# Performance work log

Hardware: AMD Instinct MI355X
Metric: run time of the kernel (lower is better)

## Reference

```python
import jax, jax.numpy as jnp
import numpy as np

B, NCH, T = 16, 64, 15000
WS, ST = 500, 250
SR = 250.0
EPS = 1e-06
DM = 512
LN_EPS = 1e-05


def _spectral_constants():
    freqs = np.fft.rfftfreq(WS, d=1.0 / SR).astype(np.float32)  # [F]
    bands = [(1.0, 4.0), (4.0, 8.0), (8.0, 13.0), (13.0, 30.0)]
    bm = np.stack([(freqs >= lo) & (freqs < hi) for lo, hi in bands]).astype(np.float32)  # [4, F]
    bm_norm = bm / bm.sum(axis=1, keepdims=True)  # mean over band bins == matmul with normalized mask
    alpha = ((freqs >= 7.0) & (freqs <= 13.5)).astype(np.float32)  # [F]
    return jnp.asarray(freqs), jnp.asarray(bm_norm), jnp.asarray(alpha)

FREQS, BAND_MASK_NORM, ALPHA_MASK = _spectral_constants()
NUM_FRAMES = (T - WS) // ST + 1
FRAME_IDX = np.arange(NUM_FRAMES)[:, None] * ST + np.arange(WS)[None, :]  # [W, WS]


def _linear_params(k, fin, fout):
    kw, kb = jax.random.split(k)
    W = jax.random.normal(kw, (fin, fout), jnp.float32) * 0.02
    b = jax.random.normal(kb, (fout,), jnp.float32) * 0.01
    return W, b


def setup_inputs() -> dict:
    key = jax.random.key(0)
    ks = jax.random.split(key, 8)
    x = jax.random.normal(ks[0], (B, NCH, T), jnp.float32)
    sensor_pos = jax.random.normal(ks[1], (B, NCH, 2), jnp.float32) * 0.1
    sensor_mask = jax.random.bernoulli(ks[2], 0.9, (B, NCH))
    IN_F = 4 * 3 + 3   # 15
    IN_D = 4 * 2 + 3   # 11
    Wf1, bf1 = _linear_params(ks[3], IN_F, DM)
    Wf2, bf2 = _linear_params(ks[4], DM, DM)
    Wd1, bd1 = _linear_params(ks[5], IN_D, DM)
    Wd2, bd2 = _linear_params(ks[6], DM, DM)
    ln_g = jnp.ones((DM,), jnp.float32)
    ln_b = jnp.zeros((DM,), jnp.float32)
    return {"x": x, "sensor_pos": sensor_pos, "sensor_mask": sensor_mask,
            "Wf1": Wf1, "bf1": bf1, "Wf2": Wf2, "bf2": bf2,
            "ln_g": ln_g, "ln_b": ln_b,
            "Wd1": Wd1, "bd1": bd1, "Wd2": Wd2, "bd2": bd2}


def _mlp(z, W1, b1, W2, b2):
    h = jax.nn.gelu(z @ W1 + b1, approximate=False)
    return h @ W2 + b2


def _layernorm(z, g, b):
    mu = z.mean(-1, keepdims=True)
    var = jnp.var(z, axis=-1, keepdims=True)
    return (z - mu) * jax.lax.rsqrt(var + LN_EPS) * g + b


def _safe_mask(v, fallback):
    return jnp.where(v.any(), v, jnp.full_like(v, fallback))


def _forward(x, sensor_pos, sensor_mask, Wf1, bf1, Wf2, bf2, ln_g, ln_b, Wd1, bd1, Wd2, bd2):
    # frames: [B, W, C, WS]
    frames = x[:, :, FRAME_IDX].transpose(0, 2, 1, 3)
    frames = frames - frames.mean(-1, keepdims=True)
    valid = sensor_mask.astype(frames.dtype)[:, None, :, None]  # [B,1,C,1]
    frames = frames * valid
    spec = jnp.fft.rfft(frames.astype(jnp.float32), axis=-1)
    power = jnp.abs(spec) ** 2 + EPS  # [B,W,C,F]

    # masked band-power means via normalized mask matmul -> [B,W,C,4]
    band_power_t = jnp.einsum('bwcf,kf->bwck', power, BAND_MASK_NORM)
    total_power = jnp.maximum(band_power_t.sum(-1, keepdims=True), EPS)
    rel_power = band_power_t / total_power

    valid_ch = valid  # [B,1,C,1]
    ch_cnt = jnp.maximum(valid_ch.sum(2, keepdims=True), 1.0)
    chan_mean = (band_power_t * valid_ch).sum(2, keepdims=True) / ch_cnt
    topo_dev = jnp.log(jnp.maximum(band_power_t, EPS)) - jnp.log(jnp.maximum(chan_mean, EPS))

    pos_x = sensor_pos[..., 0]
    pos_y = sensor_pos[..., 1]
    left = _safe_mask((pos_x < -0.02) & sensor_mask, False)
    right = _safe_mask((pos_x > 0.02) & sensor_mask, False)
    posterior = _safe_mask((pos_y < -0.02) & sensor_mask, True)
    anterior = _safe_mask((pos_y > 0.02) & sensor_mask, False)

    alpha_power = band_power_t[..., 2]  # [B,W,C]

    def region_mean(m):  # m: [B,C] bool -> [B,W]
        cnt = jnp.maximum(m.sum(-1).astype(alpha_power.dtype), 1.0)[:, None]
        return (alpha_power * m.astype(alpha_power.dtype)[:, None, :]).sum(-1) / cnt

    left_a, right_a = region_mean(left), region_mean(right)
    post_a, ant_a = region_mean(posterior), region_mean(anterior)
    alpha_asym = (left_a - right_a) / jnp.maximum(left_a + right_a + EPS, EPS)
    alpha_ap = (post_a - ant_a) / jnp.maximum(post_a + ant_a + EPS, EPS)
    support = (anterior.sum(-1) > 0) & (posterior.sum(-1) > 0)  # [B]
    alpha_ap = jnp.where(support[:, None], alpha_ap, jnp.zeros_like(alpha_ap))

    alpha_spec = power * ALPHA_MASK  # [B,W,C,F]
    alpha_sum = jnp.maximum(alpha_spec.sum(-1), EPS)
    alpha_peak_freq = (alpha_spec * FREQS).sum(-1) / alpha_sum  # [B,W,C]
    alpha_peak_score = alpha_spec.max(-1) / jnp.maximum(power.mean(-1), EPS)

    log_power = jnp.log(jnp.maximum(band_power_t, EPS))
    channel_ap = jnp.broadcast_to(sensor_pos[:, None, :, 1], alpha_peak_freq.shape)

    features = jnp.concatenate([
        log_power, rel_power, topo_dev,
        alpha_peak_freq[..., None], alpha_peak_score[..., None], channel_ap[..., None],
    ], axis=-1)  # [B,W,C,15]

    ch_cnt2 = jnp.maximum(valid_ch.sum(2), 1.0)  # [B,1,1]
    band_mean = (band_power_t * valid_ch).sum(2) / ch_cnt2       # [B,W,4]
    band_rel_mean = (rel_power * valid_ch).sum(2) / ch_cnt2      # [B,W,4]
    band_log_mean = jnp.log(jnp.maximum(band_mean, EPS))
    delta_theta = band_rel_mean[..., 0] + band_rel_mean[..., 1]
    desc = jnp.concatenate([
        band_log_mean, band_rel_mean,
        jnp.stack([alpha_asym, alpha_ap, delta_theta], axis=-1),
    ], axis=-1)  # [B,W,11]

    tokens = _layernorm(_mlp(features.astype(x.dtype), Wf1, bf1, Wf2, bf2), ln_g, ln_b)
    desc_out = _mlp(desc.astype(x.dtype), Wd1, bd1, Wd2, bd2)
    return tokens, desc_out


def reference(x, sensor_pos, sensor_mask, Wf1, bf1, Wf2, bf2, ln_g, ln_b, Wd1, bd1, Wd2, bd2):
    return _forward(x, sensor_pos, sensor_mask, Wf1, bf1, Wf2, bf2, ln_g, ln_b, Wd1, bd1, Wd2, bd2)
```

## Files before the change

### kernel.cpp

```cpp
#include <hip/hip_runtime.h>
#include <math.h>

#define EPS 1e-6f
#define LN_EPS 1e-5f

typedef __attribute__((ext_vector_type(8))) short bf16x8;
typedef __attribute__((ext_vector_type(4))) float f32x4;

#define SD_OFF    0ULL
#define SD_SZ     (1024ULL*60*128*4)
#define BP_OFF    SD_OFF
#define BTH_OFF   (SD_OFF + 4ULL*1024*1024)
#define BTL_OFF   (BTH_OFF + 65536ULL)
#define FEAT_OFF  (SD_OFF + SD_SZ)
#define FEAT_SZ   (60416ULL*16*4)
#define W1H_OFF   (FEAT_OFF + FEAT_SZ)
#define W1L_OFF   (W1H_OFF + 32768ULL)
#define WT_OFF    (W1L_OFF + 32768ULL)
#define WT_SZ     (512ULL*512*2)
#define DSC_OFF   (WT_OFF + WT_SZ)
#define DSC_SZ    (944ULL*16*4)
#define MSK_OFF   (DSC_OFF + DSC_SZ)
#define MSK_SZ    (1024ULL*4)
#define REG_OFF   (MSK_OFF + MSK_SZ)
#define REG_SZ    (4096ULL*4)
#define CNT_OFF   (REG_OFF + REG_SZ)
#define CNT_SZ    (64ULL*4)
#define SUP_OFF   (CNT_OFF + CNT_SZ)

#define TOKENS_N  30932992ULL

__device__ inline unsigned short f2bf(float f) {
  union { float f; unsigned u; } v; v.f = f;
  unsigned u = v.u;
  return (unsigned short)((u + 0x7fffu + ((u >> 16) & 1u)) >> 16);
}

__device__ inline void gload16(const void* g, void* l) {
  __builtin_amdgcn_global_load_lds((const __attribute__((address_space(1))) unsigned int*)g,
                                   (__attribute__((address_space(3))) unsigned int*)l, 16, 0, 0);
}

__global__ __launch_bounds__(1024) void k_setup(const void* mraw, const float* spos,
    float* maskf, float* regm, float* cnts, float* sup) {
  __shared__ int okint, okflt;
  __shared__ int anyr[4];
  __shared__ float cbuf[4][16];
  int t = threadIdx.x;
  if (t == 0) { okint = 1; okflt = 1; }
  if (t < 4) anyr[t] = 0;
  if (t < 64) cbuf[t>>4][t&15] = 0.f;
  __syncthreads();
  if (t < 256) {
    unsigned v = ((const unsigned*)mraw)[t];
    if (v > 1u) okint = 0;
    if (v != 0u && v != 0x3f800000u) okflt = 0;
  }
  __syncthreads();
  float mv;
  if (okint)      mv = (float)((const int*)mraw)[t];
  else if (okflt) mv = ((const float*)mraw)[t];
  else            mv = (float)((const unsigned char*)mraw)[t];
  maskf[t] = mv;
  bool mk = mv > 0.5f;
  float px = spos[2*t], py = spos[2*t+1];
  int lm = ((px < -0.02f) && mk) ? 1 : 0;
  int rm = ((px >  0.02f) && mk) ? 1 : 0;
  int pm = ((py < -0.02f) && mk) ? 1 : 0;
  int am = ((py >  0.02f) && mk) ? 1 : 0;
  if (lm) anyr[0] = 1;
  if (rm) anyr[1] = 1;
  if (pm) anyr[2] = 1;
  if (am) anyr[3] = 1;
  __syncthreads();
  float lv = anyr[0] ? (float)lm : 0.f;
  float rv = anyr[1] ? (float)rm : 0.f;
  float pv = anyr[2] ? (float)pm : 1.f;
  float av = anyr[3] ? (float)am : 0.f;
  regm[t] = lv; regm[1024+t] = rv; regm[2048+t] = pv; regm[3072+t] = av;
  int b = t >> 6;
  atomicAdd(&cbuf[0][b], lv);
  atomicAdd(&cbuf[1][b], rv);
  atomicAdd(&cbuf[2][b], pv);
  atomicAdd(&cbuf[3][b], av);
  __syncthreads();
  if (t < 64) cnts[t] = cbuf[t>>4][t&15];
  if (t < 16) sup[t] = (cbuf[3][t] > 0.f && cbuf[2][t] > 0.f) ? 1.f : 0.f;
}

__global__ __launch_bounds__(256) void k_wt(const float* Wf2, unsigned short* Wt) {
  __shared__ float tile[64][65];
  int tx = threadIdx.x & 63, ty = threadIdx.x >> 6;
  int k0 = blockIdx.x * 64, n0 = blockIdx.y * 64;
  for (int r = ty; r < 64; r += 4)
    tile[r][tx] = Wf2[(size_t)(k0 + r)*512 + n0 + tx];
  __syncthreads();
  for (int r = ty; r < 64; r += 4)
    Wt[(size_t)(n0 + r)*512 + k0 + tx] = f2bf(tile[tx][r]);
}

__global__ __launch_bounds__(256) void k_w1(const float* Wf1, unsigned short* W1h, unsigned short* W1l) {
  int id = blockIdx.x*256 + threadIdx.x;
  int col = id & 511, k = id >> 9;
  float w = (k < 15) ? Wf1[k*512 + col] : 0.f;
  unsigned u = __float_as_uint(w);
  float hf = __uint_as_float(u & 0xffff0000u);
  float r = w - hf;
  int idx = (((col >> 4)*4 + (k >> 3))*16 + (col & 15))*8 + (k & 7);
  W1h[idx] = (unsigned short)(u >> 16);
  W1l[idx] = (unsigned short)(__float_as_uint(r) >> 16);
}

__global__ __launch_bounds__(256) void k_twid(unsigned short* FBh, unsigned short* FBl) {
  int col = blockIdx.x, k = threadIdx.x;
  float w = 0.f;
  if (k < 250) {
    if (col < 116) {
      int kk = (col >> 1) + 2;
      int km = (kk * k) % 500;
      float ang = (float)km * 0.012566370614359172f;
      w = (col & 1) ? sinf(ang) : cosf(ang);
    } else if (col == 116) w = (k & 1) ? -1.f : 1.f;
    else if (col == 117) w = 1.f;
  }
  unsigned u = __float_as_uint(w);
  float hf = __uint_as_float(u & 0xffff0000u);
  float r = w - hf;
  int ni2 = col >> 6, nf = (col >> 4) & 3, r15 = col & 15;
  int kt = k >> 5, lg4 = (k >> 3) & 3, e = k & 7;
  int idx = ((((kt*2 + ni2)*4 + nf)*64) + (lg4*16 + r15))*8 + e;
  FBh[idx] = (unsigned short)(u >> 16);
  FBl[idx] = (unsigned short)(__float_as_uint(r) >> 16);
}

__global__ __launch_bounds__(256) void k_dft(const float* __restrict__ x, const float* maskf,
    const unsigned short* __restrict__ FBh, const unsigned short* __restrict__ FBl,
    float* __restrict__ bpg) {
  int c = blockIdx.x, b = blockIdx.y;
  int bc = b*64 + c;
  __shared__ __align__(16) float xs[15360];
  __shared__ float Ep[64][4];
  int t = threadIdx.x;
  float mvv = maskf[bc];
  const float4* xp4 = (const float4*)(x + (size_t)bc*15000);
  float4* xs4 = (float4*)xs;
  for (int i = t; i < 3750; i += 256) {
    float4 v = xp4[i];
    v.x *= mvv; v.y *= mvv; v.z *= mvv; v.w *= mvv;
    xs4[i] = v;
  }
  if (t < 90) xs4[3750 + t] = make_float4(0.f, 0.f, 0.f, 0.f);
  __syncthreads();
  if (t < 240) {
    int j = t >> 2, q = t & 3;
    int len = (q < 3) ? 31 : 32;
    const float2* p = (const float2*)(xs + j*250 + q*62);
    float e = 0.f;
    for (int i = 0; i < len; ++i) { float2 v = p[i]; e = fmaf(v.x, v.x, fmaf(v.y, v.y, e)); }
    Ep[j][q] = e;
  }
  int L = t & 63, wv = t >> 6;
  int mi2 = wv >> 1, ni2 = wv & 1;
  int r15 = L & 15, lg4 = L >> 4;
  f32x4 acc[2][4];
#pragma unroll
  for (int mf = 0; mf < 2; ++mf)
#pragma unroll
    for (int nf = 0; nf < 4; ++nf) acc[mf][nf] = (f32x4){0.f,0.f,0.f,0.f};
  int rowA = mi2*32 + r15;
  const unsigned short* fbh0 = FBh + (size_t)(ni2*4*64 + L)*8;
  const unsigned short* fbl0 = FBl + (size_t)(ni2*4*64 + L)*8;
  for (int kt = 0; kt < 8; ++kt) {
    int k0 = kt*32 + lg4*8;
    bf16x8 bh[4], bl[4];
#pragma unroll
    for (int nf = 0; nf < 4; ++nf) {
      bh[nf] = *(const bf16x8*)(fbh0 + (size_t)(kt*8 + nf)*512);
      bl[nf] = *(const bf16x8*)(fbl0 + (size_t)(kt*8 + nf)*512);
    }
    bf16x8 ah[2], al[2];
#pragma unroll
    for (int mf = 0; mf < 2; ++mf) {
      int row = rowA + mf*16;
      if (row > 60) row = 60;
      int base = row*250 + k0;
      float v[8];
#pragma unroll
      for (int p = 0; p < 4; ++p) {
        float2 vv = *(const float2*)(xs + base + 2*p);
        v[2*p] = vv.x; v[2*p+1] = vv.y;
      }
#pragma unroll
      for (int e = 0; e < 8; ++e) {
        unsigned u = __float_as_uint(v[e]);
        float hf = __uint_as_float(u & 0xffff0000u);
        ah[mf][e] = (short)(u >> 16);
        al[mf][e] = (short)(__float_as_uint(v[e] - hf) >> 16);
      }
    }
#pragma unroll
    for (int mf = 0; mf < 2; ++mf)
#pragma unroll
      for (int nf = 0; nf < 4; ++nf) {
        acc[mf][nf] = __builtin_amdgcn_mfma_f32_16x16x32_bf16(ah[mf], bh[nf], acc[mf][nf], 0, 0, 0);
        acc[mf][nf] = __builtin_amdgcn_mfma_f32_16x16x32_bf16(al[mf], bh[nf], acc[mf][nf], 0, 0, 0);
        acc[mf][nf] = __builtin_amdgcn_mfma_f32_16x16x32_bf16(ah[mf], bl[nf], acc[mf][nf], 0, 0, 0);
      }
  }
  __syncthreads();
  float* Ts = xs;
#pragma unroll
  for (int mf = 0; mf < 2; ++mf)
#pragma unroll
    for (int nf = 0; nf < 4; ++nf) {
      int col = ni2*64 + nf*16 + r15;
      int rw = mi2*32 + mf*16 + lg4*4;
#pragma unroll
      for (int q = 0; q < 4; ++q) Ts[(rw + q)*129 + col] = acc[mf][nf][q];
    }
  __syncthreads();
  if (t < 59) {
    int w = t;
    const float* r0 = Ts + w*129;
    const float* r1 = Ts + (w+1)*129;
    float bs0=0,bs1=0,bs2=0,bs3=0, asum=0, afsum=0, amax=0;
#pragma unroll
    for (int i = 0; i < 58; ++i) {
      float sg = (i & 1) ? -1.f : 1.f;
      float tc = fmaf(sg, r1[2*i],   r0[2*i]);
      float ts = fmaf(sg, r1[2*i+1], r0[2*i+1]);
      float P = fmaf(tc, tc, fmaf(ts, ts, EPS));
      if (i < 6) bs0 += P; else if (i < 14) bs1 += P; else if (i < 24) bs2 += P; else bs3 += P;
      if (i >= 12 && i <= 25) { asum += P; afsum = fmaf(P, 0.5f*(float)(i+2), afsum); amax = fmaxf(amax, P); }
    }
    float nyq  = r0[116] + r1[116];
    float ssum = r0[117] + r1[117];
    float en = Ep[w][0]+Ep[w][1]+Ep[w][2]+Ep[w][3] + Ep[w+1][0]+Ep[w+1][1]+Ep[w+1][2]+Ep[w+1][3];
    float E = fmaf(-ssum * (1.f/500.f), ssum, en);
    float pmean = fmaxf(fmaf(500.f, E, nyq*nyq) * (1.f/502.f) + EPS, EPS);
    float bp0 = bs0*(1.f/6.f), bp1 = bs1*(1.f/8.f), bp2 = bs2*(1.f/10.f), bp3 = bs3*(1.f/34.f);
    float afreq  = afsum / fmaxf(asum, EPS);
    float ascore = amax / pmean;
    float4* o = (float4*)(bpg + (((size_t)(b*59 + w))*64 + c)*8);
    o[0] = make_float4(bp0, bp1, bp2, bp3);
    o[1] = make_float4(afreq, ascore, 0.f, 0.f);
  }
}

__global__ __launch_bounds__(64) void k_feat2(const float* __restrict__ bpg, const float* spos,
    const float* maskf, const float* regm, const float* cnts, const float* sup,
    float* feat, float* descb) {
  int w = blockIdx.x, b = blockIdx.y;
  int c = threadIdx.x, bc = b*64 + c;
  size_t bw = (size_t)(b*59 + w);
  const float4* ip = (const float4*)(bpg + (bw*64 + c)*8);
  float4 f0 = ip[0], f1 = ip[1];
  float bp0 = f0.x, bp1 = f0.y, bp2 = f0.z, bp3 = f0.w;
  float tot = fmaxf(bp0+bp1+bp2+bp3, EPS);
  float rl0 = bp0/tot, rl1 = bp1/tot, rl2 = bp2/tot, rl3 = bp3/tot;
  float valid = maskf[bc];
  float vcnt = valid;
  float ch0 = bp0*valid, ch1 = bp1*valid, ch2 = bp2*valid, ch3 = bp3*valid;
  float br0 = rl0*valid, br1 = rl1*valid, br2 = rl2*valid, br3 = rl3*valid;
  float rg0 = bp2*regm[bc], rg1 = bp2*regm[1024+bc], rg2 = bp2*regm[2048+bc], rg3 = bp2*regm[3072+bc];
#pragma unroll
  for (int off = 1; off < 64; off <<= 1) {
    vcnt += __shfl_xor(vcnt, off, 64);
    ch0 += __shfl_xor(ch0, off, 64); ch1 += __shfl_xor(ch1, off, 64);
    ch2 += __shfl_xor(ch2, off, 64); ch3 += __shfl_xor(ch3, off, 64);
    br0 += __shfl_xor(br0, off, 64); br1 += __shfl_xor(br1, off, 64);
    br2 += __shfl_xor(br2, off, 64); br3 += __shfl_xor(br3, off, 64);
    rg0 += __shfl_xor(rg0, off, 64); rg1 += __shfl_xor(rg1, off, 64);
    rg2 += __shfl_xor(rg2, off, 64); rg3 += __shfl_xor(rg3, off, 64);
  }
  float ccnt = fmaxf(vcnt, 1.f);
  float cm0 = ch0/ccnt, cm1 = ch1/ccnt, cm2 = ch2/ccnt, cm3 = ch3/ccnt;
  float lcm0 = logf(fmaxf(cm0,EPS)), lcm1 = logf(fmaxf(cm1,EPS));
  float lcm2 = logf(fmaxf(cm2,EPS)), lcm3 = logf(fmaxf(cm3,EPS));
  float lg0 = logf(fmaxf(bp0,EPS)), lg1 = logf(fmaxf(bp1,EPS));
  float lg2 = logf(fmaxf(bp2,EPS)), lg3 = logf(fmaxf(bp3,EPS));
  float* fr = feat + (bw*64 + c)*16;
  fr[0]=lg0; fr[1]=lg1; fr[2]=lg2; fr[3]=lg3;
  fr[4]=rl0; fr[5]=rl1; fr[6]=rl2; fr[7]=rl3;
  fr[8]=lg0-lcm0; fr[9]=lg1-lcm1; fr[10]=lg2-lcm2; fr[11]=lg3-lcm3;
  fr[12]=f1.x;
  fr[13]=f1.y;
  fr[14]=spos[bc*2 + 1];
  fr[15]=0.f;
  if (c == 0) {
    float bR0 = br0/ccnt, bR1 = br1/ccnt, bR2 = br2/ccnt, bR3 = br3/ccnt;
    float Lm = rg0 / fmaxf(cnts[b],      1.f);
    float Rm = rg1 / fmaxf(cnts[16+b],   1.f);
    float Pm = rg2 / fmaxf(cnts[32+b],   1.f);
    float Am = rg3 / fmaxf(cnts[48+b],   1.f);
    float* dr = descb + bw*16;
    dr[0]=lcm0; dr[1]=lcm1; dr[2]=lcm2; dr[3]=lcm3;
    dr[4]=bR0; dr[5]=bR1; dr[6]=bR2; dr[7]=bR3;
    dr[8]=(Lm - Rm) / fmaxf(Lm + Rm + EPS, EPS);
    dr[9]=(sup[b] > 0.5f) ? (Pm - Am) / fmaxf(Pm + Am + EPS, EPS) : 0.f;
    dr[10]=bR0 + bR1;
  }
}

__global__ __launch_bounds__(256, 2) void k_tok(const float* __restrict__ feat,
    const unsigned short* __restrict__ W1h, const unsigned short* __restrict__ W1l,
    const float* __restrict__ bf1, const unsigned short* __restrict__ Wt,
    const float* bf2, const float* lng, const float* lnb, float* out) {
  __shared__ __align__(16) unsigned short As[64*32];
  __shared__ __align__(16) unsigned short Bs[512*32];
  __shared__ float b1s[512];
  __shared__ float red[64][4][2];
  __shared__ float lnp[64][2];
  int t = threadIdx.x;
  int L = t & 63, wvid = t >> 6;
  int row0 = blockIdx.x * 64;
  int r15 = L & 15, lg4 = L >> 4;
  if (t < 256) { b1s[t] = bf1[t]; b1s[256+t] = bf1[256+t]; }
  bf16x8 a1h = (bf16x8){0,0,0,0,0,0,0,0}, a1l = (bf16x8){0,0,0,0,0,0,0,0};
  {
    int row = row0 + wvid*16 + r15;
    if (lg4 < 2) {
      const float4* fp = (const float4*)(feat + (size_t)row*16 + lg4*8);
      float4 v0 = fp[0], v1 = fp[1];
      float v[8] = {v0.x, v0.y, v0.z, v0.w, v1.x, v1.y, v1.z, v1.w};
#pragma unroll
      for (int e = 0; e < 8; ++e) {
        unsigned u = __float_as_uint(v[e]);
        float hf = __uint_as_float(u & 0xffff0000u);
        a1h[e] = (short)(u >> 16);
        a1l[e] = (short)(__float_as_uint(v[e] - hf) >> 16);
      }
    }
  }
  f32x4 acc[4][8];
#pragma unroll
  for (int m = 0; m < 4; ++m)
#pragma unroll
    for (int n = 0; n < 8; ++n) acc[m][n] = (f32x4){0.f,0.f,0.f,0.f};
  int swz = (r15 >> 1) & 3;
  int kca = lg4 ^ swz;
  int aoff = r15*32 + kca*8;
  int boff = (wvid*128 + r15)*32 + kca*8;
  __syncthreads();
  for (int kt = 0; kt < 16; ++kt) {
#pragma unroll
    for (int r = 0; r < 8; ++r) {
      int n = r*256 + t;
      int col = n >> 2;
      int kc = (n & 3) ^ ((n >> 3) & 3);
      gload16(Wt + (size_t)col*512 + kt*32 + kc*8, (char*)Bs + n*16);
    }
    f32x4 acc1[2];
    acc1[0] = (f32x4){0.f,0.f,0.f,0.f};
    acc1[1] = (f32x4){0.f,0.f,0.f,0.f};
#pragma unroll
    for (int n2 = 0; n2 < 2; ++n2) {
      const unsigned short* wb = W1h + (size_t)(kt*2 + n2)*512 + L*8;
      const unsigned short* wl = W1l + (size_t)(kt*2 + n2)*512 + L*8;
      bf16x8 b1h = *(const bf16x8*)wb;
      bf16x8 b1l = *(const bf16x8*)wl;
      acc1[n2] = __builtin_amdgcn_mfma_f32_16x16x32_bf16(a1h, b1h, acc1[n2], 0, 0, 0);
      acc1[n2] = __builtin_amdgcn_mfma_f32_16x16x32_bf16(a1l, b1h, acc1[n2], 0, 0, 0);
      acc1[n2] = __builtin_amdgcn_mfma_f32_16x16x32_bf16(a1h, b1l, acc1[n2], 0, 0, 0);
    }
    unsigned short hv[8];
#pragma unroll
    for (int n2 = 0; n2 < 2; ++n2) {
      float bb = b1s[kt*32 + n2*16 + r15];
#pragma unroll
      for (int q = 0; q < 4; ++q) {
        float z = acc1[n2][q] + bb;
        float g = 0.5f * z * (1.f + erff(z * 0.70710678118654752f));
        hv[n2*4 + q] = f2bf(g);
      }
    }
#pragma unroll
    for (int n2 = 0; n2 < 2; ++n2) {
      int col5 = n2*16 + r15;
      int cb = col5 >> 3;
#pragma unroll
      for (int q = 0; q < 4; ++q) {
        int rw = wvid*16 + lg4*4 + q;
        int kcs = cb ^ ((rw >> 1) & 3);
        As[rw*32 + kcs*8 + (col5 & 7)] = hv[n2*4 + q];
      }
    }
    __syncthreads();
    bf16x8 av[4], bv[8];
#pragma unroll
    for (int m = 0; m < 4; ++m) av[m] = *(const bf16x8*)&As[aoff + m*512];
#pragma unroll
    for (int n = 0; n < 8; ++n) bv[n] = *(const bf16x8*)&Bs[boff + n*512];
#pragma unroll
    for (int m = 0; m < 4; ++m)
#pragma unroll
      for (int n = 0; n < 8; ++n)
        acc[m][n] = __builtin_amdgcn_mfma_f32_16x16x32_bf16(av[m], bv[n], acc[m][n], 0, 0, 0);
    __syncthreads();
  }
  float b2v[8], gv[8], btv[8];
#pragma unroll
  for (int n = 0; n < 8; ++n) {
    int col = wvid*128 + n*16 + r15;
    b2v[n] = bf2[col]; gv[n] = lng[col]; btv[n] = lnb[col];
  }
  float s1[4][4], s2[4][4];
#pragma unroll
  for (int m = 0; m < 4; ++m)
#pragma unroll
    for (int r = 0; r < 4; ++r) { s1[m][r] = 0.f; s2[m][r] = 0.f; }
#pragma unroll
  for (int m = 0; m < 4; ++m)
#pragma unroll
    for (int n = 0; n < 8; ++n)
#pragma unroll
      for (int r = 0; r < 4; ++r) {
        float z = acc[m][n][r] + b2v[n];
        acc[m][n][r] = z;
        s1[m][r] += z;
        s2[m][r] = fmaf(z, z, s2[m][r]);
      }
#pragma unroll
  for (int off = 1; off < 16; off <<= 1)
#pragma unroll
    for (int m = 0; m < 4; ++m)
#pragma unroll
      for (int r = 0; r < 4; ++r) {
        s1[m][r] += __shfl_xor(s1[m][r], off, 64);
        s2[m][r] += __shfl_xor(s2[m][r], off, 64);
      }
  if (r15 == 0) {
#pragma unroll
    for (int m = 0; m < 4; ++m)
#pragma unroll
      for (int r = 0; r < 4; ++r) {
        int rw = m*16 + lg4*4 + r;
        red[rw][wvid][0] = s1[m][r];
        red[rw][wvid][1] = s2[m][r];
      }
  }
  __syncthreads();
  if (t < 64) {
    float a = red[t][0][0] + red[t][1][0] + red[t][2][0] + red[t][3][0];
    float q = red[t][0][1] + red[t][1][1] + red[t][2][1] + red[t][3][1];
    float mu = a * (1.f/512.f);
    float var = q * (1.f/512.f) - mu*mu;
    lnp[t][0] = mu;
    lnp[t][1] = rsqrtf(var + LN_EPS);
  }
  __syncthreads();
  float* ob = out + (size_t)row0*512;
#pragma unroll
  for (int m = 0; m < 4; ++m)
#pragma unroll
    for (int r = 0; r < 4; ++r) {
      int rw = m*16 + lg4*4 + r;
      float mu = lnp[rw][0], rs = lnp[rw][1];
#pragma unroll
      for (int n = 0; n < 8; ++n) {
        int col = wvid*128 + n*16 + r15;
        ob[(size_t)rw*512 + col] = fmaf((acc[m][n][r] - mu)*rs, gv[n], btv[n]);
      }
    }
}

__global__ __launch_bounds__(256) void k_desc(const float* descb, const float* Wd1, const float* bd1,
    const float* Wd2, const float* bd2, float* out) {
  int blk = blockIdx.x;
  int cq = blockIdx.y;
  __shared__ float ds[16][12];
  __shared__ float hd[16*512];
  int t = threadIdx.x;
  { int r = t >> 4, cc = t & 15;
    if (cc < 11) ds[r][cc] = descb[(size_t)(blk*16 + r)*16 + cc]; }
  __syncthreads();
  {
    int c0 = t, c1 = t + 256;
    float wa[11], wb[11];
#pragma unroll
    for (int k = 0; k < 11; ++k) { wa[k] = Wd1[k*512+c0]; wb[k] = Wd1[k*512+c1]; }
    float ba = bd1[c0], bb = bd1[c1];
    for (int r = 0; r < 16; ++r) {
      float a0 = ba, a1 = bb;
#pragma unroll
      for (int k = 0; k < 11; ++k) { float f = ds[r][k]; a0 = fmaf(f, wa[k], a0); a1 = fmaf(f, wb[k], a1); }
      hd[r*512+c0] = 0.5f * a0 * (1.f + erff(a0 * 0.70710678118654752f));
      hd[r*512+c1] = 0.5f * a1 * (1.f + erff(a1 * 0.70710678118654752f));
    }
  }
  __syncthreads();
  int col = cq*128 + (t & 127);
  int half = t >> 7;
  float accv[8];
  float bz = bd2[col];
#pragma unroll
  for (int r = 0; r < 8; ++r) accv[r] = bz;
  for (int k4 = 0; k4 < 128; ++k4) {
    float w0 = Wd2[(size_t)(k4*4+0)*512 + col];
    float w1 = Wd2[(size_t)(k4*4+1)*512 + col];
    float w2 = Wd2[(size_t)(k4*4+2)*512 + col];
    float w3 = Wd2[(size_t)(k4*4+3)*512 + col];
#pragma unroll
    for (int r = 0; r < 8; ++r) {
      float4 hv = *(const float4*)&hd[(half*8+r)*512 + k4*4];
      accv[r] = fmaf(hv.x, w0, fmaf(hv.y, w1, fmaf(hv.z, w2, fmaf(hv.w, w3, accv[r]))));
    }
  }
  float* ob = out + TOKENS_N;
#pragma unroll
  for (int r = 0; r < 8; ++r) {
    int grow = blk*16 + half*8 + r;
    ob[(size_t)grow*512 + col] = accv[r];
  }
}

extern "C" void kernel_launch(void* const* d_in, const int* in_sizes, int n_in,
                              void* d_out, int out_size, void* d_ws, size_t ws_size,
                              hipStream_t stream) {
  (void)in_sizes; (void)n_in; (void)out_size; (void)ws_size;
  const float* x    = (const float*)d_in[0];
  const float* spos = (const float*)d_in[1];
  const void*  mask = d_in[2];
  const float* Wf1  = (const float*)d_in[3];
  const float* bf1  = (const float*)d_in[4];
  const float* Wf2  = (const float*)d_in[5];
  const float* bf2  = (const float*)d_in[6];
  const float* lng  = (const float*)d_in[7];
  const float* lnb  = (const float*)d_in[8];
  const float* Wd1  = (const float*)d_in[9];
  const float* bd1  = (const float*)d_in[10];
  const float* Wd2  = (const float*)d_in[11];
  const float* bd2  = (const float*)d_in[12];
  char* ws = (char*)d_ws;
  float*          bpg   = (float*)(ws + BP_OFF);
  unsigned short* FBh   = (unsigned short*)(ws + BTH_OFF);
  unsigned short* FBl   = (unsigned short*)(ws + BTL_OFF);
  float*          feat  = (float*)(ws + FEAT_OFF);
  unsigned short* W1h   = (unsigned short*)(ws + W1H_OFF);
  unsigned short* W1l   = (unsigned short*)(ws + W1L_OFF);
  unsigned short* Wt    = (unsigned short*)(ws + WT_OFF);
  float*          descb = (float*)(ws + DSC_OFF);
  float*          maskf = (float*)(ws + MSK_OFF);
  float*          regm  = (float*)(ws + REG_OFF);
  float*          cnts  = (float*)(ws + CNT_OFF);
  float*          sup   = (float*)(ws + SUP_OFF);
  float*          out   = (float*)d_out;

  hipLaunchKernelGGL(k_setup,  dim3(1),      dim3(1024), 0, stream, mask, spos, maskf, regm, cnts, sup);
  hipLaunchKernelGGL(k_wt,     dim3(8,8),    dim3(256),  0, stream, Wf2, Wt);
  hipLaunchKernelGGL(k_w1,     dim3(64),     dim3(256),  0, stream, Wf1, W1h, W1l);
  hipLaunchKernelGGL(k_twid,   dim3(128),    dim3(256),  0, stream, FBh, FBl);
  hipLaunchKernelGGL(k_dft,    dim3(64,16),  dim3(256),  0, stream, x, maskf, FBh, FBl, bpg);
  hipLaunchKernelGGL(k_feat2,  dim3(59,16),  dim3(64),   0, stream, bpg, spos, maskf, regm, cnts, sup, feat, descb);
  hipLaunchKernelGGL(k_tok,    dim3(944),    dim3(256),  0, stream, feat, W1h, W1l, bf1, Wt, bf2, lng, lnb, out);
  hipLaunchKernelGGL(k_desc,   dim3(59,4),   dim3(256),  0, stream, descb, Wd1, bd1, Wd2, bd2, out);
}
```

Baseline: 345.3 us.

## Split k_tok into producer/consumer waves and use fast erf approximation for GELU

k_tok now runs 512 threads per block: four waves compute the first-layer MLP and GELU into LDS, while the other four issue the Wt global-to-LDS loads. Then all eight waves share the second GEMM as a 2x4 wave grid, so each wave holds half as many accumulators. GELU's erff is replaced by an Abramowitz-Stegun polynomial with a hardware reciprocal and exp, in both k_tok and k_desc. This aims to cut register pressure, raise occupancy and overlap loads with compute, at the cost of a small accuracy loss in GELU.

```diff
diff --git a/kernel.cpp b/kernel.cpp
--- a/kernel.cpp
+++ b/kernel.cpp
@@ -39,6 +39,16 @@
 __device__ inline void gload16(const void* g, void* l) {
   __builtin_amdgcn_global_load_lds((const __attribute__((address_space(1))) unsigned int*)g,
                                    (__attribute__((address_space(3))) unsigned int*)l, 16, 0, 0);
+}
+
+__device__ inline float gelu_f(float z) {
+  float s = z * 0.70710678118654752f;
+  float a = fabsf(s);
+  float t = __builtin_amdgcn_rcpf(fmaf(0.3275911f, a, 1.f));
+  float p = t*(0.254829592f + t*(-0.284496736f + t*(1.421413741f + t*(-1.453152027f + t*1.061405429f))));
+  float e = __expf(-a*a);
+  float er = copysignf(fmaf(-p, e, 1.f), s);
+  return 0.5f * z * (1.f + er);
 }
 
 __global__ __launch_bounds__(1024) void k_setup(const void* mraw, const float* spos,
@@ -302,7 +312,7 @@
   }
 }
 
-__global__ __launch_bounds__(256, 2) void k_tok(const float* __restrict__ feat,
+__global__ __launch_bounds__(512, 4) void k_tok(const float* __restrict__ feat,
     const unsigned short* __restrict__ W1h, const unsigned short* __restrict__ W1l,
     const float* __restrict__ bf1, const unsigned short* __restrict__ Wt,
     const float* bf2, const float* lng, const float* lnb, float* out) {
@@ -312,87 +322,85 @@
   __shared__ float red[64][4][2];
   __shared__ float lnp[64][2];
   int t = threadIdx.x;
-  int L = t & 63, wvid = t >> 6;
+  int L = t & 63, wv = t >> 6;
+  int wm = wv >> 2, wn = wv & 3;
   int row0 = blockIdx.x * 64;
   int r15 = L & 15, lg4 = L >> 4;
-  if (t < 256) { b1s[t] = bf1[t]; b1s[256+t] = bf1[256+t]; }
+  if (t < 512) b1s[t] = bf1[t];
   bf16x8 a1h = (bf16x8){0,0,0,0,0,0,0,0}, a1l = (bf16x8){0,0,0,0,0,0,0,0};
-  {
-    int row = row0 + wvid*16 + r15;
-    if (lg4 < 2) {
-      const float4* fp = (const float4*)(feat + (size_t)row*16 + lg4*8);
-      float4 v0 = fp[0], v1 = fp[1];
-      float v[8] = {v0.x, v0.y, v0.z, v0.w, v1.x, v1.y, v1.z, v1.w};
-#pragma unroll
-      for (int e = 0; e < 8; ++e) {
-        unsigned u = __float_as_uint(v[e]);
-        float hf = __uint_as_float(u & 0xffff0000u);
-        a1h[e] = (short)(u >> 16);
-        a1l[e] = (short)(__float_as_uint(v[e] - hf) >> 16);
-      }
-    }
-  }
-  f32x4 acc[4][8];
-#pragma unroll
-  for (int m = 0; m < 4; ++m)
+  if (wv < 4 && lg4 < 2) {
+    int row = row0 + wv*16 + r15;
+    const float4* fp = (const float4*)(feat + (size_t)row*16 + lg4*8);
+    float4 v0 = fp[0], v1 = fp[1];
+    float v[8] = {v0.x, v0.y, v0.z, v0.w, v1.x, v1.y, v1.z, v1.w};
+#pragma unroll
+    for (int e = 0; e < 8; ++e) {
+      unsigned u = __float_as_uint(v[e]);
+      float hf = __uint_as_float(u & 0xffff0000u);
+      a1h[e] = (short)(u >> 16);
+      a1l[e] = (short)(__float_as_uint(v[e] - hf) >> 16);
+    }
+  }
+  f32x4 acc[2][8];
+#pragma unroll
+  for (int m = 0; m < 2; ++m)
 #pragma unroll
     for (int n = 0; n < 8; ++n) acc[m][n] = (f32x4){0.f,0.f,0.f,0.f};
   int swz = (r15 >> 1) & 3;
   int kca = lg4 ^ swz;
-  int aoff = r15*32 + kca*8;
-  int boff = (wvid*128 + r15)*32 + kca*8;
   __syncthreads();
   for (int kt = 0; kt < 16; ++kt) {
-#pragma unroll
-    for (int r = 0; r < 8; ++r) {
-      int n = r*256 + t;
-      int col = n >> 2;
-      int kc = (n & 3) ^ ((n >> 3) & 3);
-      gload16(Wt + (size_t)col*512 + kt*32 + kc*8, (char*)Bs + n*16);
-    }
-    f32x4 acc1[2];
-    acc1[0] = (f32x4){0.f,0.f,0.f,0.f};
-    acc1[1] = (f32x4){0.f,0.f,0.f,0.f};
-#pragma unroll
-    for (int n2 = 0; n2 < 2; ++n2) {
-      const unsigned short* wb = W1h + (size_t)(kt*2 + n2)*512 + L*8;
-      const unsigned short* wl = W1l + (size_t)(kt*2 + n2)*512 + L*8;
-      bf16x8 b1h = *(const bf16x8*)wb;
-      bf16x8 b1l = *(const bf16x8*)wl;
-      acc1[n2] = __builtin_amdgcn_mfma_f32_16x16x32_bf16(a1h, b1h, acc1[n2], 0, 0, 0);
-      acc1[n2] = __builtin_amdgcn_mfma_f32_16x16x32_bf16(a1l, b1h, acc1[n2], 0, 0, 0);
-      acc1[n2] = __builtin_amdgcn_mfma_f32_16x16x32_bf16(a1h, b1l, acc1[n2], 0, 0, 0);
-    }
-    unsigned short hv[8];
-#pragma unroll
-    for (int n2 = 0; n2 < 2; ++n2) {
-      float bb = b1s[kt*32 + n2*16 + r15];
-#pragma unroll
-      for (int q = 0; q < 4; ++q) {
-        float z = acc1[n2][q] + bb;
-        float g = 0.5f * z * (1.f + erff(z * 0.70710678118654752f));
-        hv[n2*4 + q] = f2bf(g);
-      }
-    }
-#pragma unroll
-    for (int n2 = 0; n2 < 2; ++n2) {
-      int col5 = n2*16 + r15;
-      int cb = col5 >> 3;
-#pragma unroll
-      for (int q = 0; q < 4; ++q) {
-        int rw = wvid*16 + lg4*4 + q;
-        int kcs = cb ^ ((rw >> 1) & 3);
-        As[rw*32 + kcs*8 + (col5 & 7)] = hv[n2*4 + q];
+    if (wv >= 4) {
+      int ts = t - 256;
+#pragma unroll
+      for (int r = 0; r < 8; ++r) {
+        int n = r*256 + ts;
+        int col = n >> 2;
+        int kc = (n & 3) ^ ((n >> 3) & 3);
+        gload16(Wt + (size_t)col*512 + kt*32 + kc*8, (char*)Bs + n*16);
+      }
+    } else {
+      f32x4 acc1[2];
+      acc1[0] = (f32x4){0.f,0.f,0.f,0.f};
+      acc1[1] = (f32x4){0.f,0.f,0.f,0.f};
+#pragma unroll
+      for (int n2 = 0; n2 < 2; ++n2) {
+        bf16x8 b1h = *(const bf16x8*)(W1h + (size_t)(kt*2 + n2)*512 + L*8);
+        bf16x8 b1l = *(const bf16x8*)(W1l + (size_t)(kt*2 + n2)*512 + L*8);
+        acc1[n2] = __builtin_amdgcn_mfma_f32_16x16x32_bf16(a1h, b1h, acc1[n2], 0, 0, 0);
+        acc1[n2] = __builtin_amdgcn_mfma_f32_16x16x32_bf16(a1l, b1h, acc1[n2], 0, 0, 0);
+        acc1[n2] = __builtin_amdgcn_mfma_f32_16x16x32_bf16(a1h, b1l, acc1[n2], 0, 0, 0);
+      }
+      unsigned short hv[8];
+#pragma unroll
+      for (int n2 = 0; n2 < 2; ++n2) {
+        float bb = b1s[kt*32 + n2*16 + r15];
+#pragma unroll
+        for (int q = 0; q < 4; ++q)
+          hv[n2*4 + q] = f2bf(gelu_f(acc1[n2][q] + bb));
+      }
+#pragma unroll
+      for (int n2 = 0; n2 < 2; ++n2) {
+        int col5 = n2*16 + r15;
+        int cb = col5 >> 3;
+#pragma unroll
+        for (int q = 0; q < 4; ++q) {
+          int rw = wv*16 + lg4*4 + q;
+          int kcs = cb ^ ((rw >> 1) & 3);
+          As[rw*32 + kcs*8 + (col5 & 7)] = hv[n2*4 + q];
+        }
       }
     }
     __syncthreads();
-    bf16x8 av[4], bv[8];
-#pragma unroll
-    for (int m = 0; m < 4; ++m) av[m] = *(const bf16x8*)&As[aoff + m*512];
-#pragma unroll
-    for (int n = 0; n < 8; ++n) bv[n] = *(const bf16x8*)&Bs[boff + n*512];
-#pragma unroll
-    for (int m = 0; m < 4; ++m)
+    bf16x8 av[2], bv[8];
+#pragma unroll
+    for (int m = 0; m < 2; ++m)
+      av[m] = *(const bf16x8*)&As[(wm*32 + m*16 + r15)*32 + kca*8];
+#pragma unroll
+    for (int n = 0; n < 8; ++n)
+      bv[n] = *(const bf16x8*)&Bs[(wn*128 + n*16 + r15)*32 + kca*8];
+#pragma unroll
+    for (int m = 0; m < 2; ++m)
 #pragma unroll
       for (int n = 0; n < 8; ++n)
         acc[m][n] = __builtin_amdgcn_mfma_f32_16x16x32_bf16(av[m], bv[n], acc[m][n], 0, 0, 0);
@@ -401,16 +409,16 @@
   float b2v[8], gv[8], btv[8];
 #pragma unroll
   for (int n = 0; n < 8; ++n) {
-    int col = wvid*128 + n*16 + r15;
+    int col = wn*128 + n*16 + r15;
     b2v[n] = bf2[col]; gv[n] = lng[col]; btv[n] = lnb[col];
   }
-  float s1[4][4], s2[4][4];
-#pragma unroll
-  for (int m = 0; m < 4; ++m)
+  float s1[2][4], s2[2][4];
+#pragma unroll
+  for (int m = 0; m < 2; ++m)
 #pragma unroll
     for (int r = 0; r < 4; ++r) { s1[m][r] = 0.f; s2[m][r] = 0.f; }
 #pragma unroll
-  for (int m = 0; m < 4; ++m)
+  for (int m = 0; m < 2; ++m)
 #pragma unroll
     for (int n = 0; n < 8; ++n)
 #pragma unroll
@@ -423,7 +431,7 @@
 #pragma unroll
   for (int off = 1; off < 16; off <<= 1)
 #pragma unroll
-    for (int m = 0; m < 4; ++m)
+    for (int m = 0; m < 2; ++m)
 #pragma unroll
       for (int r = 0; r < 4; ++r) {
         s1[m][r] += __shfl_xor(s1[m][r], off, 64);
@@ -431,12 +439,12 @@
       }
   if (r15 == 0) {
 #pragma unroll
-    for (int m = 0; m < 4; ++m)
+    for (int m = 0; m < 2; ++m)
 #pragma unroll
       for (int r = 0; r < 4; ++r) {
-        int rw = m*16 + lg4*4 + r;
-        red[rw][wvid][0] = s1[m][r];
-        red[rw][wvid][1] = s2[m][r];
+        int rw = wm*32 + m*16 + lg4*4 + r;
+        red[rw][wn][0] = s1[m][r];
+        red[rw][wn][1] = s2[m][r];
       }
   }
   __syncthreads();
@@ -451,14 +459,14 @@
   __syncthreads();
   float* ob = out + (size_t)row0*512;
 #pragma unroll
-  for (int m = 0; m < 4; ++m)
+  for (int m = 0; m < 2; ++m)
 #pragma unroll
     for (int r = 0; r < 4; ++r) {
-      int rw = m*16 + lg4*4 + r;
+      int rw = wm*32 + m*16 + lg4*4 + r;
       float mu = lnp[rw][0], rs = lnp[rw][1];
 #pragma unroll
       for (int n = 0; n < 8; ++n) {
-        int col = wvid*128 + n*16 + r15;
+        int col = wn*128 + n*16 + r15;
         ob[(size_t)rw*512 + col] = fmaf((acc[m][n][r] - mu)*rs, gv[n], btv[n]);
       }
     }
@@ -484,8 +492,8 @@
       float a0 = ba, a1 = bb;
 #pragma unroll
       for (int k = 0; k < 11; ++k) { float f = ds[r][k]; a0 = fmaf(f, wa[k], a0); a1 = fmaf(f, wb[k], a1); }
-      hd[r*512+c0] = 0.5f * a0 * (1.f + erff(a0 * 0.70710678118654752f));
-      hd[r*512+c1] = 0.5f * a1 * (1.f + erff(a1 * 0.70710678118654752f));
+      hd[r*512+c0] = gelu_f(a0);
+      hd[r*512+c1] = gelu_f(a1);
     }
   }
   __syncthreads();
@@ -552,6 +560,6 @@
   hipLaunchKernelGGL(k_twid,   dim3(128),    dim3(256),  0, stream, FBh, FBl);
   hipLaunchKernelGGL(k_dft,    dim3(64,16),  dim3(256),  0, stream, x, maskf, FBh, FBl, bpg);
   hipLaunchKernelGGL(k_feat2,  dim3(59,16),  dim3(64),   0, stream, bpg, spos, maskf, regm, cnts, sup, feat, descb);
-  hipLaunchKernelGGL(k_tok,    dim3(944),    dim3(256),  0, stream, feat, W1h, W1l, bf1, Wt, bf2, lng, lnb, out);
+  hipLaunchKernelGGL(k_tok,    dim3(944),    dim3(512),  0, stream, feat, W1h, W1l, bf1, Wt, bf2, lng, lnb, out);
   hipLaunchKernelGGL(k_desc,   dim3(59,4),   dim3(256),  0, stream, descb, Wd1, bd1, Wd2, bd2, out);
 }
```

Result: slower. 380.5 us (+10.2%).

## Double-buffer token MLP tiles and use a fast erf approximation in GELU

Applied to the files above, without the earlier changes.

The k_tok loop now keeps two LDS buffers for the W2 tile and the GELU hidden tile. Each iteration stages the next tile's async loads and computes its first-layer GELU while the current tile's MFMAs run, which removes one barrier per iteration. Exact erff in GELU is replaced everywhere by an Abramowitz-Stegun polynomial using rcp and exp, which cuts transcendental cost. The trade-offs are double the LDS use, which may limit two blocks per CU, and slightly lower GELU accuracy (about 1e-7 abs error, masked by the bf16 rounding).

```diff
diff --git a/kernel.cpp b/kernel.cpp
--- a/kernel.cpp
+++ b/kernel.cpp
@@ -39,6 +39,16 @@
 __device__ inline void gload16(const void* g, void* l) {
   __builtin_amdgcn_global_load_lds((const __attribute__((address_space(1))) unsigned int*)g,
                                    (__attribute__((address_space(3))) unsigned int*)l, 16, 0, 0);
+}
+
+__device__ inline float gelu_f(float z) {
+  float s = z * 0.70710678118654752f;
+  float a = fabsf(s);
+  float t = __builtin_amdgcn_rcpf(fmaf(0.3275911f, a, 1.f));
+  float p = t*(0.254829592f + t*(-0.284496736f + t*(1.421413741f + t*(-1.453152027f + t*1.061405429f))));
+  float e = __expf(-a*a);
+  float er = copysignf(fmaf(-p, e, 1.f), s);
+  return 0.5f * z * (1.f + er);
 }
 
 __global__ __launch_bounds__(1024) void k_setup(const void* mraw, const float* spos,
@@ -306,8 +316,8 @@
     const unsigned short* __restrict__ W1h, const unsigned short* __restrict__ W1l,
     const float* __restrict__ bf1, const unsigned short* __restrict__ Wt,
     const float* bf2, const float* lng, const float* lnb, float* out) {
-  __shared__ __align__(16) unsigned short As[64*32];
-  __shared__ __align__(16) unsigned short Bs[512*32];
+  __shared__ __align__(16) unsigned short As[2][64*32];
+  __shared__ __align__(16) unsigned short Bs[2][512*32];
   __shared__ float b1s[512];
   __shared__ float red[64][4][2];
   __shared__ float lnp[64][2];
@@ -315,21 +325,19 @@
   int L = t & 63, wvid = t >> 6;
   int row0 = blockIdx.x * 64;
   int r15 = L & 15, lg4 = L >> 4;
-  if (t < 256) { b1s[t] = bf1[t]; b1s[256+t] = bf1[256+t]; }
+  { b1s[t] = bf1[t]; b1s[256+t] = bf1[256+t]; }
   bf16x8 a1h = (bf16x8){0,0,0,0,0,0,0,0}, a1l = (bf16x8){0,0,0,0,0,0,0,0};
-  {
+  if (lg4 < 2) {
     int row = row0 + wvid*16 + r15;
-    if (lg4 < 2) {
-      const float4* fp = (const float4*)(feat + (size_t)row*16 + lg4*8);
-      float4 v0 = fp[0], v1 = fp[1];
-      float v[8] = {v0.x, v0.y, v0.z, v0.w, v1.x, v1.y, v1.z, v1.w};
-#pragma unroll
-      for (int e = 0; e < 8; ++e) {
-        unsigned u = __float_as_uint(v[e]);
-        float hf = __uint_as_float(u & 0xffff0000u);
-        a1h[e] = (short)(u >> 16);
-        a1l[e] = (short)(__float_as_uint(v[e] - hf) >> 16);
-      }
+    const float4* fp = (const float4*)(feat + (size_t)row*16 + lg4*8);
+    float4 v0 = fp[0], v1 = fp[1];
+    float v[8] = {v0.x, v0.y, v0.z, v0.w, v1.x, v1.y, v1.z, v1.w};
+#pragma unroll
+    for (int e = 0; e < 8; ++e) {
+      unsigned u = __float_as_uint(v[e]);
+      float hf = __uint_as_float(u & 0xffff0000u);
+      a1h[e] = (short)(u >> 16);
+      a1l[e] = (short)(__float_as_uint(v[e] - hf) >> 16);
     }
   }
   f32x4 acc[4][8];
@@ -341,56 +349,58 @@
   int kca = lg4 ^ swz;
   int aoff = r15*32 + kca*8;
   int boff = (wvid*128 + r15)*32 + kca*8;
-  __syncthreads();
+
+#define STAGE_BS(KT, BUF) do { \
+    _Pragma("unroll") \
+    for (int r_ = 0; r_ < 8; ++r_) { \
+      int n_ = r_*256 + t; \
+      int col_ = n_ >> 2; \
+      int kc_ = (n_ & 3) ^ ((n_ >> 3) & 3); \
+      gload16(Wt + (size_t)col_*512 + (KT)*32 + kc_*8, (char*)&Bs[BUF][0] + n_*16); \
+    } } while (0)
+
+#define JIT_H(KT, BUF) do { \
+    f32x4 acc1_[2]; \
+    acc1_[0] = (f32x4){0.f,0.f,0.f,0.f}; \
+    acc1_[1] = (f32x4){0.f,0.f,0.f,0.f}; \
+    _Pragma("unroll") \
+    for (int n2_ = 0; n2_ < 2; ++n2_) { \
+      bf16x8 b1h_ = *(const bf16x8*)(W1h + (size_t)((KT)*2 + n2_)*512 + L*8); \
+      bf16x8 b1l_ = *(const bf16x8*)(W1l + (size_t)((KT)*2 + n2_)*512 + L*8); \
+      acc1_[n2_] = __builtin_amdgcn_mfma_f32_16x16x32_bf16(a1h, b1h_, acc1_[n2_], 0, 0, 0); \
+      acc1_[n2_] = __builtin_amdgcn_mfma_f32_16x16x32_bf16(a1l, b1h_, acc1_[n2_], 0, 0, 0); \
+      acc1_[n2_] = __builtin_amdgcn_mfma_f32_16x16x32_bf16(a1h, b1l_, acc1_[n2_], 0, 0, 0); \
+    } \
+    _Pragma("unroll") \
+    for (int n2_ = 0; n2_ < 2; ++n2_) { \
+      float bb_ = b1s[(KT)*32 + n2_*16 + r15]; \
+      int col5_ = n2_*16 + r15; \
+      int cb_ = col5_ >> 3; \
+      _Pragma("unroll") \
+      for (int q_ = 0; q_ < 4; ++q_) { \
+        float z_ = acc1_[n2_][q_] + bb_; \
+        int rw_ = wvid*16 + lg4*4 + q_; \
+        int kcs_ = cb_ ^ ((rw_ >> 1) & 3); \
+        As[BUF][rw_*32 + kcs_*8 + (col5_ & 7)] = f2bf(gelu_f(z_)); \
+      } \
+    } } while (0)
+
+  STAGE_BS(0, 0);
+  __syncthreads();
+  JIT_H(0, 0);
+  __syncthreads();
+
   for (int kt = 0; kt < 16; ++kt) {
-#pragma unroll
-    for (int r = 0; r < 8; ++r) {
-      int n = r*256 + t;
-      int col = n >> 2;
-      int kc = (n & 3) ^ ((n >> 3) & 3);
-      gload16(Wt + (size_t)col*512 + kt*32 + kc*8, (char*)Bs + n*16);
-    }
-    f32x4 acc1[2];
-    acc1[0] = (f32x4){0.f,0.f,0.f,0.f};
-    acc1[1] = (f32x4){0.f,0.f,0.f,0.f};
-#pragma unroll
-    for (int n2 = 0; n2 < 2; ++n2) {
-      const unsigned short* wb = W1h + (size_t)(kt*2 + n2)*512 + L*8;
-      const unsigned short* wl = W1l + (size_t)(kt*2 + n2)*512 + L*8;
-      bf16x8 b1h = *(const bf16x8*)wb;
-      bf16x8 b1l = *(const bf16x8*)wl;
-      acc1[n2] = __builtin_amdgcn_mfma_f32_16x16x32_bf16(a1h, b1h, acc1[n2], 0, 0, 0);
-      acc1[n2] = __builtin_amdgcn_mfma_f32_16x16x32_bf16(a1l, b1h, acc1[n2], 0, 0, 0);
-      acc1[n2] = __builtin_amdgcn_mfma_f32_16x16x32_bf16(a1h, b1l, acc1[n2], 0, 0, 0);
-    }
-    unsigned short hv[8];
-#pragma unroll
-    for (int n2 = 0; n2 < 2; ++n2) {
-      float bb = b1s[kt*32 + n2*16 + r15];
-#pragma unroll
-      for (int q = 0; q < 4; ++q) {
-        float z = acc1[n2][q] + bb;
-        float g = 0.5f * z * (1.f + erff(z * 0.70710678118654752f));
-        hv[n2*4 + q] = f2bf(g);
-      }
-    }
-#pragma unroll
-    for (int n2 = 0; n2 < 2; ++n2) {
-      int col5 = n2*16 + r15;
-      int cb = col5 >> 3;
-#pragma unroll
-      for (int q = 0; q < 4; ++q) {
-        int rw = wvid*16 + lg4*4 + q;
-        int kcs = cb ^ ((rw >> 1) & 3);
-        As[rw*32 + kcs*8 + (col5 & 7)] = hv[n2*4 + q];
-      }
-    }
-    __syncthreads();
+    int cur = kt & 1, nxt = cur ^ 1;
+    if (kt < 15) {
+      STAGE_BS(kt+1, nxt);
+      JIT_H(kt+1, nxt);
+    }
     bf16x8 av[4], bv[8];
 #pragma unroll
-    for (int m = 0; m < 4; ++m) av[m] = *(const bf16x8*)&As[aoff + m*512];
-#pragma unroll
-    for (int n = 0; n < 8; ++n) bv[n] = *(const bf16x8*)&Bs[boff + n*512];
+    for (int m = 0; m < 4; ++m) av[m] = *(const bf16x8*)&As[cur][aoff + m*512];
+#pragma unroll
+    for (int n = 0; n < 8; ++n) bv[n] = *(const bf16x8*)&Bs[cur][boff + n*512];
 #pragma unroll
     for (int m = 0; m < 4; ++m)
 #pragma unroll
@@ -398,6 +408,9 @@
         acc[m][n] = __builtin_amdgcn_mfma_f32_16x16x32_bf16(av[m], bv[n], acc[m][n], 0, 0, 0);
     __syncthreads();
   }
+#undef STAGE_BS
+#undef JIT_H
+
   float b2v[8], gv[8], btv[8];
 #pragma unroll
   for (int n = 0; n < 8; ++n) {
@@ -484,8 +497,8 @@
       float a0 = ba, a1 = bb;
 #pragma unroll
       for (int k = 0; k < 11; ++k) { float f = ds[r][k]; a0 = fmaf(f, wa[k], a0); a1 = fmaf(f, wb[k], a1); }
-      hd[r*512+c0] = 0.5f * a0 * (1.f + erff(a0 * 0.70710678118654752f));
-      hd[r*512+c1] = 0.5f * a1 * (1.f + erff(a1 * 0.70710678118654752f));
+      hd[r*512+c0] = gelu_f(a0);
+      hd[r*512+c1] = gelu_f(a1);
     }
   }
   __syncthreads();
```

Result: no change. 339.1 us (-1.8%).
